# Optimization experiments

Hardware: AMD Instinct MI355X
Metric: run time of the kernel (lower is better)

## Reference

```python
import jax, jax.numpy as jnp
import numpy as np

N_COMPANIES = 2000
HIDDEN = 256
HEADS = 8
LAYERS = 3
IN_DIM = 64
NEG_SLOPE = 0.2  # PyG GATConv default leaky_relu slope


def setup_inputs() -> dict:
    key = jax.random.key(0)
    ks = jax.random.split(key, 32)
    B, E = 64, 64000
    C = HIDDEN // HEADS
    emb_dim = HIDDEN // 4
    def lin(k, fo, fi):
        k1, k2 = jax.random.split(k)
        s = 1.0 / np.sqrt(fi)
        return (jax.random.uniform(k1, (fo, fi), jnp.float32, -s, s),
                jax.random.uniform(k2, (fo,), jnp.float32, -s, s))
    inp = {}
    inp['x'] = jax.random.normal(ks[0], (B, IN_DIM), jnp.float32)
    inp['company_indices'] = jax.random.randint(ks[1], (B,), 0, N_COMPANIES)
    inp['edge_index'] = jax.random.randint(ks[2], (2, E), 0, N_COMPANIES)
    inp['edge_attr'] = jax.random.uniform(ks[3], (E,), jnp.float32)
    inp['W_in'], inp['b_in'] = lin(ks[4], HIDDEN, IN_DIM)
    # stacked GAT params (all layers same shape)
    g = 0.05
    inp['gat_W'] = g * jax.random.normal(ks[5], (LAYERS, HEADS * C, HIDDEN), jnp.float32)
    inp['gat_att_src'] = g * jax.random.normal(ks[6], (LAYERS, HEADS, C), jnp.float32)
    inp['gat_att_dst'] = g * jax.random.normal(ks[7], (LAYERS, HEADS, C), jnp.float32)
    inp['gat_We'] = g * jax.random.normal(ks[8], (LAYERS, HEADS * C, 1), jnp.float32)
    inp['gat_att_edge'] = g * jax.random.normal(ks[9], (LAYERS, HEADS, C), jnp.float32)
    inp['gat_b'] = jnp.zeros((LAYERS, HEADS * C), jnp.float32)
    inp['emb'] = jax.random.normal(ks[10], (N_COMPANIES, emb_dim), jnp.float32)
    inp['W_fuse'], inp['b_fuse'] = lin(ks[11], HIDDEN, HIDDEN + emb_dim)
    inp['W_p1'], inp['b_p1'] = lin(ks[12], HIDDEN // 2, HIDDEN)
    inp['W_p2'], inp['b_p2'] = lin(ks[13], HIDDEN // 4, HIDDEN // 2)
    inp['W_p3'], inp['b_p3'] = lin(ks[14], 1, HIDDEN // 4)
    inp['W_d1'], inp['b_d1'] = lin(ks[15], HIDDEN // 2, HIDDEN)
    inp['W_d2'], inp['b_d2'] = lin(ks[16], HIDDEN // 4, HIDDEN // 2)
    inp['W_d3'], inp['b_d3'] = lin(ks[17], 1, HIDDEN // 4)
    return inp


def _gat_layer(xg, src, dst, ea, W, att_s, att_d, We, att_e, b, N):
    # xg: [N, F] node features; src/dst: [E2] (with self-loops); ea: [E2]
    H, C = att_s.shape
    xp = (xg @ W.T).reshape(N, H, C)
    a_s = jnp.sum(xp * att_s, -1)                       # [N, H]
    a_d = jnp.sum(xp * att_d, -1)                       # [N, H]
    ef = (ea[:, None] @ We.T).reshape(-1, H, C)         # [E2, H, C]
    a_e = jnp.sum(ef * att_e, -1)                       # [E2, H]
    logits = jax.nn.leaky_relu(a_s[src] + a_d[dst] + a_e, NEG_SLOPE)
    m = jax.ops.segment_max(logits, dst, num_segments=N)
    ex = jnp.exp(logits - m[dst])
    denom = jax.ops.segment_sum(ex, dst, num_segments=N)
    alpha = ex / (denom[dst] + 1e-16)                   # per-dst softmax
    out = jax.ops.segment_sum(alpha[:, :, None] * xp[src], dst, num_segments=N)
    return out.reshape(N, H * C) + b


def reference(x, company_indices, edge_index, edge_attr, W_in, b_in,
              gat_W, gat_att_src, gat_att_dst, gat_We, gat_att_edge, gat_b,
              emb, W_fuse, b_fuse, W_p1, b_p1, W_p2, b_p2, W_p3, b_p3,
              W_d1, b_d1, W_d2, b_d2, W_d3, b_d3):
    # eval mode: dropout is identity
    B = x.shape[0]
    N = emb.shape[0]
    h = jax.nn.relu(x @ W_in.T + b_in)                  # [B, hidden]
    # add self loops (PyG default, fill_value='mean' for edge_attr)
    loops = jnp.arange(N, dtype=edge_index.dtype)
    src = jnp.concatenate([edge_index[0], loops])
    dst = jnp.concatenate([edge_index[1], loops])
    ea = jnp.concatenate([edge_attr, jnp.full((N,), edge_attr.mean(), edge_attr.dtype)])

    def per_item(hi):
        g = jnp.broadcast_to(hi, (N, hi.shape[0]))
        for l in range(gat_W.shape[0]):
            g = jax.nn.relu(_gat_layer(g, src, dst, ea, gat_W[l], gat_att_src[l],
                                       gat_att_dst[l], gat_We[l], gat_att_edge[l], gat_b[l], N))
        return g

    gouts = jax.vmap(per_item)(h)                       # [B, N, hidden]
    comp_out = gouts[jnp.arange(B), company_indices]    # [B, hidden]
    comp_emb = emb[company_indices]                     # [B, hidden//4]
    fused = jax.nn.relu(jnp.concatenate([comp_out, comp_emb], -1) @ W_fuse.T + b_fuse)
    p = jax.nn.relu(fused @ W_p1.T + b_p1)
    p = jax.nn.relu(p @ W_p2.T + b_p2)
    price = (p @ W_p3.T + b_p3).squeeze(-1)
    d = jax.nn.relu(fused @ W_d1.T + b_d1)
    d = jax.nn.relu(d @ W_d2.T + b_d2)
    direction = jax.nn.sigmoid((d @ W_d3.T + b_d3)).squeeze(-1)
    return price, direction
```

## Files before the change

kernel.cpp:

```cpp
#include <hip/hip_runtime.h>
#include <math.h>


#define B_ITEMS 64

typedef _Float16 half_t;
typedef _Float16 half8 __attribute__((ext_vector_type(8)));

#define OFF_WIN   0
#define OFF_GAT   16384
#define OFF_FUSE  212992
#define OFF_P1    294912
#define OFF_D1    327680
#define OFF_P2    360448
#define OFF_D2    368640
#define TOT_W     376832

#define BIN   0
#define BGAT  256
#define BFUSE 1024
#define BP1   1280
#define BD1   1408
#define BP2   1536
#define BD2   1600
#define NBIAS 1664

extern "C" __global__ __launch_bounds__(1024) void compress_w(
    const float* __restrict__ W_in, const float* __restrict__ gat_W,
    const float* __restrict__ W_fuse, const float* __restrict__ W_p1,
    const float* __restrict__ W_d1, const float* __restrict__ W_p2,
    const float* __restrict__ W_d2, half_t* __restrict__ ws)
{
    const int e = (blockIdx.x * 1024 + threadIdx.x) * 8;
    const float* src;
    int off;
    if      (e < OFF_GAT)  { src = W_in;   off = e; }
    else if (e < OFF_FUSE) { src = gat_W;  off = e - OFF_GAT; }
    else if (e < OFF_P1)   { src = W_fuse; off = e - OFF_FUSE; }
    else if (e < OFF_D1)   { src = W_p1;   off = e - OFF_P1; }
    else if (e < OFF_P2)   { src = W_d1;   off = e - OFF_D1; }
    else if (e < OFF_D2)   { src = W_p2;   off = e - OFF_P2; }
    else                   { src = W_d2;   off = e - OFF_D2; }
    const float4* s4 = reinterpret_cast<const float4*>(src + off);
    float4 a = s4[0], b = s4[1];
    half8 h = { (_Float16)a.x, (_Float16)a.y, (_Float16)a.z, (_Float16)a.w,
                (_Float16)b.x, (_Float16)b.y, (_Float16)b.z, (_Float16)b.w };
    *reinterpret_cast<half8*>(ws + e) = h;
}

template <int K, int G>
struct WFrag { half8 w[K / (8 * G)]; };

template <int K, int G>
__device__ __forceinline__ void load_frag(WFrag<K, G>& f,
                                          const half_t* __restrict__ Wh, int t) {
    const int c = t & (G - 1);
    const int o = t / G;
    const half8* __restrict__ W8 =
        reinterpret_cast<const half8*>(Wh + (size_t)o * K);
#pragma unroll
    for (int j = 0; j < K / (8 * G); ++j) f.w[j] = W8[j * G + c];
}

template <int M, int K, int G>
__device__ __forceinline__ void compute_frag(const WFrag<K, G>& f,
                                             const float* __restrict__ bias,
                                             const float* __restrict__ in,
                                             float* __restrict__ out,
                                             int t) {
    const int c = t & (G - 1);
    const int o = t / G;
    const float4* __restrict__ A4 = reinterpret_cast<const float4*>(in);
    float acc = 0.f;
#pragma unroll
    for (int j = 0; j < K / (8 * G); ++j) {
        const int idx = j * G + c;
        float4 a0 = A4[2 * idx];
        float4 a1 = A4[2 * idx + 1];
        half8 w = f.w[j];
        acc = fmaf((float)w[0], a0.x, acc);
        acc = fmaf((float)w[1], a0.y, acc);
        acc = fmaf((float)w[2], a0.z, acc);
        acc = fmaf((float)w[3], a0.w, acc);
        acc = fmaf((float)w[4], a1.x, acc);
        acc = fmaf((float)w[5], a1.y, acc);
        acc = fmaf((float)w[6], a1.z, acc);
        acc = fmaf((float)w[7], a1.w, acc);
    }
#pragma unroll
    for (int s = 1; s < G; s <<= 1) acc += __shfl_xor(acc, s, 64);
    if (c == 0) out[o] = fmaxf(acc + bias[o], 0.f);
}

extern "C" __global__ __launch_bounds__(1024) void fin_gat_v6(
    const float* __restrict__ x,
    const int* __restrict__ cidx,
    const half_t* __restrict__ ws,
    const float* __restrict__ b_in,
    const float* __restrict__ gat_b,
    const float* __restrict__ emb,
    const float* __restrict__ b_fuse,
    const float* __restrict__ b_p1,
    const float* __restrict__ b_p2,
    const float* __restrict__ W_p3, const float* __restrict__ b_p3,
    const float* __restrict__ b_d1,
    const float* __restrict__ b_d2,
    const float* __restrict__ W_d3, const float* __restrict__ b_d3,
    float* __restrict__ out)
{
    __shared__ float bufA[320];
    __shared__ float bufB[320];
    __shared__ float bias_lds[NBIAS];

    const int b = blockIdx.x;
    const int t = threadIdx.x;

    WFrag<64, 4> f_in;
    load_frag(f_in, ws + OFF_WIN, t);

    if (t < 64) {
        const int ci = cidx[b];
        bufA[t] = x[b * 64 + t];
        bufA[256 + t] = emb[(size_t)ci * 64 + t];
    }
    float wdot = 0.f, bdot = 0.f;
    if (t < 64)            wdot = W_p3[t];
    else if (t < 128)      wdot = W_d3[t - 64];
    if (t == 0)            bdot = b_p3[0];
    else if (t == 64)      bdot = b_d3[0];

#pragma unroll
    for (int i = t; i < NBIAS; i += 1024) {
        float v;
        if      (i < 256)  v = b_in[i];
        else if (i < 1024) v = gat_b[i - 256];
        else if (i < 1280) v = b_fuse[i - 1024];
        else if (i < 1408) v = b_p1[i - 1280];
        else if (i < 1536) v = b_d1[i - 1408];
        else if (i < 1600) v = b_p2[i - 1536];
        else               v = b_d2[i - 1600];
        bias_lds[i] = v;
    }
    __syncthreads();

    WFrag<256, 4> fg0;
    load_frag(fg0, ws + OFF_GAT + 0 * 65536, t);
    compute_frag<256, 64, 4>(f_in, bias_lds + BIN, bufA, bufB, t);
    __syncthreads();

    WFrag<256, 4> fg1;
    load_frag(fg1, ws + OFF_GAT + 1 * 65536, t);
    compute_frag<256, 256, 4>(fg0, bias_lds + BGAT, bufB, bufA, t);
    __syncthreads();

    WFrag<256, 4> fg2;
    load_frag(fg2, ws + OFF_GAT + 2 * 65536, t);
    compute_frag<256, 256, 4>(fg1, bias_lds + BGAT + 256, bufA, bufB, t);
    __syncthreads();

    WFrag<320, 4> f_fu;
    load_frag(f_fu, ws + OFF_FUSE, t);
    compute_frag<256, 256, 4>(fg2, bias_lds + BGAT + 512, bufB, bufA, t);
    __syncthreads();

    WFrag<256, 4> f_h1;
    load_frag(f_h1, (t < 512) ? ws + OFF_P1 : ws + OFF_D1, t & 511);
    compute_frag<256, 320, 4>(f_fu, bias_lds + BFUSE, bufA, bufB, t);
    __syncthreads();

    WFrag<128, 8> f_h2;
    load_frag(f_h2, (t < 512) ? ws + OFF_P2 : ws + OFF_D2, t & 511);
    if (t < 512) compute_frag<128, 256, 4>(f_h1, bias_lds + BP1, bufB, bufA, t);
    else         compute_frag<128, 256, 4>(f_h1, bias_lds + BD1, bufB, bufA + 192, t - 512);
    __syncthreads();

    if (t < 512) compute_frag<64, 128, 8>(f_h2, bias_lds + BP2, bufA, bufB, t);
    else         compute_frag<64, 128, 8>(f_h2, bias_lds + BD2, bufA + 192, bufB + 64, t - 512);
    __syncthreads();

    if (t < 64) {
        float v = wdot * bufB[t];
#pragma unroll
        for (int off = 32; off > 0; off >>= 1) v += __shfl_down(v, off, 64);
        if (t == 0) out[b] = v + bdot;
    } else if (t < 128) {
        const int u = t - 64;
        float v = wdot * bufB[64 + u];
#pragma unroll
        for (int off = 32; off > 0; off >>= 1) v += __shfl_down(v, off, 64);
        if (u == 0) {
            float z = v + bdot;
            out[B_ITEMS + b] = 1.0f / (1.0f + expf(-z));
        }
    }
}

extern "C" void kernel_launch(void* const* d_in, const int* in_sizes, int n_in,
                              void* d_out, int out_size, void* d_ws, size_t ws_size,
                              hipStream_t stream) {
    const float* x      = (const float*)d_in[0];
    const int*   cidx   = (const int*)  d_in[1];
    const float* W_in   = (const float*)d_in[4];
    const float* b_in   = (const float*)d_in[5];
    const float* gat_W  = (const float*)d_in[6];
    const float* gat_b  = (const float*)d_in[11];
    const float* emb    = (const float*)d_in[12];
    const float* W_fuse = (const float*)d_in[13];
    const float* b_fuse = (const float*)d_in[14];
    const float* W_p1   = (const float*)d_in[15];
    const float* b_p1   = (const float*)d_in[16];
    const float* W_p2   = (const float*)d_in[17];
    const float* b_p2   = (const float*)d_in[18];
    const float* W_p3   = (const float*)d_in[19];
    const float* b_p3   = (const float*)d_in[20];
    const float* W_d1   = (const float*)d_in[21];
    const float* b_d1   = (const float*)d_in[22];
    const float* W_d2   = (const float*)d_in[23];
    const float* b_d2   = (const float*)d_in[24];
    const float* W_d3   = (const float*)d_in[25];
    const float* b_d3   = (const float*)d_in[26];

    half_t* ws = (half_t*)d_ws;

    compress_w<<<46, 1024, 0, stream>>>(W_in, gat_W, W_fuse, W_p1, W_d1,
                                        W_p2, W_d2, ws);

    fin_gat_v6<<<B_ITEMS, 1024, 0, stream>>>(
        x, cidx, ws, b_in, gat_b, emb, b_fuse,
        b_p1, b_p2, W_p3, b_p3, b_d1, b_d2, W_d3, b_d3,
        (float*)d_out);
}
```

Baseline: 116.6 us.

## Fuse weight fp16 conversion into main kernel with grid-wide flag barrier

Drops the separate compress_w launch. Each of the 64 blocks now converts its own slice of the fp32 weights to fp16 in the workspace, sets a per-block flag, then spins until all 64 flags are set before reading the shared fp16 weights. Weight fragment loads are also moved one stage further ahead of the compute that uses them, so more loads are in flight. The flags are never reset and rely on the workspace starting zeroed, so on repeated calls the barrier passes at once. That could let blocks read weights before they are rewritten, and it costs extra registers for the deeper prefetch.

```diff
diff --git a/kernel.cpp b/kernel.cpp
--- a/kernel.cpp
+++ b/kernel.cpp
@@ -15,6 +15,7 @@
 #define OFF_P2    360448
 #define OFF_D2    368640
 #define TOT_W     376832
+#define CHUNKS_PER_BLOCK (TOT_W / 8 / B_ITEMS)
 
 #define BIN   0
 #define BGAT  256
@@ -24,29 +25,6 @@
 #define BP2   1536
 #define BD2   1600
 #define NBIAS 1664
-
-extern "C" __global__ __launch_bounds__(1024) void compress_w(
-    const float* __restrict__ W_in, const float* __restrict__ gat_W,
-    const float* __restrict__ W_fuse, const float* __restrict__ W_p1,
-    const float* __restrict__ W_d1, const float* __restrict__ W_p2,
-    const float* __restrict__ W_d2, half_t* __restrict__ ws)
-{
-    const int e = (blockIdx.x * 1024 + threadIdx.x) * 8;
-    const float* src;
-    int off;
-    if      (e < OFF_GAT)  { src = W_in;   off = e; }
-    else if (e < OFF_FUSE) { src = gat_W;  off = e - OFF_GAT; }
-    else if (e < OFF_P1)   { src = W_fuse; off = e - OFF_FUSE; }
-    else if (e < OFF_D1)   { src = W_p1;   off = e - OFF_P1; }
-    else if (e < OFF_P2)   { src = W_d1;   off = e - OFF_D1; }
-    else if (e < OFF_D2)   { src = W_p2;   off = e - OFF_P2; }
-    else                   { src = W_d2;   off = e - OFF_D2; }
-    const float4* s4 = reinterpret_cast<const float4*>(src + off);
-    float4 a = s4[0], b = s4[1];
-    half8 h = { (_Float16)a.x, (_Float16)a.y, (_Float16)a.z, (_Float16)a.w,
-                (_Float16)b.x, (_Float16)b.y, (_Float16)b.z, (_Float16)b.w };
-    *reinterpret_cast<half8*>(ws + e) = h;
-}
 
 template <int K, int G>
 struct WFrag { half8 w[K / (8 * G)]; };
@@ -92,20 +70,23 @@
     if (c == 0) out[o] = fmaxf(acc + bias[o], 0.f);
 }
 
-extern "C" __global__ __launch_bounds__(1024) void fin_gat_v6(
+extern "C" __global__ __launch_bounds__(1024) void fin_gat_v9(
     const float* __restrict__ x,
     const int* __restrict__ cidx,
-    const half_t* __restrict__ ws,
+    const float* __restrict__ W_in,
     const float* __restrict__ b_in,
+    const float* __restrict__ gat_W,
     const float* __restrict__ gat_b,
     const float* __restrict__ emb,
+    const float* __restrict__ W_fuse,
     const float* __restrict__ b_fuse,
-    const float* __restrict__ b_p1,
-    const float* __restrict__ b_p2,
+    const float* __restrict__ W_p1, const float* __restrict__ b_p1,
+    const float* __restrict__ W_p2, const float* __restrict__ b_p2,
     const float* __restrict__ W_p3, const float* __restrict__ b_p3,
-    const float* __restrict__ b_d1,
-    const float* __restrict__ b_d2,
+    const float* __restrict__ W_d1, const float* __restrict__ b_d1,
+    const float* __restrict__ W_d2, const float* __restrict__ b_d2,
     const float* __restrict__ W_d3, const float* __restrict__ b_d3,
+    half_t* __restrict__ ws,
     float* __restrict__ out)
 {
     __shared__ float bufA[320];
@@ -114,9 +95,25 @@
 
     const int b = blockIdx.x;
     const int t = threadIdx.x;
-
-    WFrag<64, 4> f_in;
-    load_frag(f_in, ws + OFF_WIN, t);
+    int* __restrict__ flags = (int*)(ws + TOT_W);
+
+    if (t < CHUNKS_PER_BLOCK) {
+        const int e = (b * CHUNKS_PER_BLOCK + t) * 8;
+        const float* src;
+        int off;
+        if      (e < OFF_GAT)  { src = W_in;   off = e; }
+        else if (e < OFF_FUSE) { src = gat_W;  off = e - OFF_GAT; }
+        else if (e < OFF_P1)   { src = W_fuse; off = e - OFF_FUSE; }
+        else if (e < OFF_D1)   { src = W_p1;   off = e - OFF_P1; }
+        else if (e < OFF_P2)   { src = W_d1;   off = e - OFF_D1; }
+        else if (e < OFF_D2)   { src = W_p2;   off = e - OFF_P2; }
+        else                   { src = W_d2;   off = e - OFF_D2; }
+        const float4* s4 = reinterpret_cast<const float4*>(src + off);
+        float4 a0 = s4[0], a1 = s4[1];
+        half8 h = { (_Float16)a0.x, (_Float16)a0.y, (_Float16)a0.z, (_Float16)a0.w,
+                    (_Float16)a1.x, (_Float16)a1.y, (_Float16)a1.z, (_Float16)a1.w };
+        *reinterpret_cast<half8*>(ws + e) = h;
+    }
 
     if (t < 64) {
         const int ci = cidx[b];
@@ -141,35 +138,54 @@
         else               v = b_d2[i - 1600];
         bias_lds[i] = v;
     }
-    __syncthreads();
-
+
+    __syncthreads();
+    if (t == 0) {
+        __threadfence();
+        __hip_atomic_store(&flags[b], 1, __ATOMIC_RELEASE, __HIP_MEMORY_SCOPE_AGENT);
+    }
+    if (t < 64) {
+        while (true) {
+            int v = __hip_atomic_load(&flags[t], __ATOMIC_RELAXED,
+                                      __HIP_MEMORY_SCOPE_AGENT);
+            if (__all(v == 1)) break;
+            __builtin_amdgcn_s_sleep(16);
+        }
+    }
+    __syncthreads();
+    __threadfence();
+
+    WFrag<64, 4> f_in;
+    load_frag(f_in, ws + OFF_WIN, t);
     WFrag<256, 4> fg0;
     load_frag(fg0, ws + OFF_GAT + 0 * 65536, t);
-    compute_frag<256, 64, 4>(f_in, bias_lds + BIN, bufA, bufB, t);
     __syncthreads();
 
     WFrag<256, 4> fg1;
     load_frag(fg1, ws + OFF_GAT + 1 * 65536, t);
-    compute_frag<256, 256, 4>(fg0, bias_lds + BGAT, bufB, bufA, t);
+    compute_frag<256, 64, 4>(f_in, bias_lds + BIN, bufA, bufB, t);
     __syncthreads();
 
     WFrag<256, 4> fg2;
     load_frag(fg2, ws + OFF_GAT + 2 * 65536, t);
-    compute_frag<256, 256, 4>(fg1, bias_lds + BGAT + 256, bufA, bufB, t);
+    compute_frag<256, 256, 4>(fg0, bias_lds + BGAT, bufB, bufA, t);
     __syncthreads();
 
     WFrag<320, 4> f_fu;
     load_frag(f_fu, ws + OFF_FUSE, t);
-    compute_frag<256, 256, 4>(fg2, bias_lds + BGAT + 512, bufB, bufA, t);
+    compute_frag<256, 256, 4>(fg1, bias_lds + BGAT + 256, bufA, bufB, t);
     __syncthreads();
 
     WFrag<256, 4> f_h1;
     load_frag(f_h1, (t < 512) ? ws + OFF_P1 : ws + OFF_D1, t & 511);
-    compute_frag<256, 320, 4>(f_fu, bias_lds + BFUSE, bufA, bufB, t);
+    compute_frag<256, 256, 4>(fg2, bias_lds + BGAT + 512, bufB, bufA, t);
     __syncthreads();
 
     WFrag<128, 8> f_h2;
     load_frag(f_h2, (t < 512) ? ws + OFF_P2 : ws + OFF_D2, t & 511);
+    compute_frag<256, 320, 4>(f_fu, bias_lds + BFUSE, bufA, bufB, t);
+    __syncthreads();
+
     if (t < 512) compute_frag<128, 256, 4>(f_h1, bias_lds + BP1, bufB, bufA, t);
     else         compute_frag<128, 256, 4>(f_h1, bias_lds + BD1, bufB, bufA + 192, t - 512);
     __syncthreads();
@@ -220,13 +236,9 @@
     const float* W_d3   = (const float*)d_in[25];
     const float* b_d3   = (const float*)d_in[26];
 
-    half_t* ws = (half_t*)d_ws;
-
-    compress_w<<<46, 1024, 0, stream>>>(W_in, gat_W, W_fuse, W_p1, W_d1,
-                                        W_p2, W_d2, ws);
-
-    fin_gat_v6<<<B_ITEMS, 1024, 0, stream>>>(
-        x, cidx, ws, b_in, gat_b, emb, b_fuse,
-        b_p1, b_p2, W_p3, b_p3, b_d1, b_d2, W_d3, b_d3,
-        (float*)d_out);
-}
+    fin_gat_v9<<<B_ITEMS, 1024, 0, stream>>>(
+        x, cidx, W_in, b_in, gat_W, gat_b, emb, W_fuse, b_fuse,
+        W_p1, b_p1, W_p2, b_p2, W_p3, b_p3,
+        W_d1, b_d1, W_d2, b_d2, W_d3, b_d3,
+        (half_t*)d_ws, (float*)d_out);
+}
```

Result: slower. 133.5 us (+14.6%).
